# Performance work log

Measured on AMD Instinct MI355X. Metric: run time of the kernel, lower is better.

## Reference

```python
import jax, jax.numpy as jnp
import numpy as np

EPS = 1e-08


def setup_inputs() -> dict:
    key = jax.random.key(0)
    B, D = 8192, 512
    student_output = jax.random.normal(key, (B, D), dtype=jnp.float32)
    return {"student_output": student_output}


def reference(student_output) -> jnp.ndarray:
    # F.normalize(p=2, dim=-1, eps=EPS): x / max(||x||, eps)
    norm = jnp.linalg.norm(student_output, axis=-1, keepdims=True)
    x = student_output / jnp.maximum(norm, EPS)

    n = x.shape[0]
    # Pairwise inner products; mask the diagonal with -1 (self-match)
    dots = jnp.matmul(x, x.T)  # [B, B]
    idx = jnp.arange(n)
    dots = dots.at[idx, idx].set(-1.0)
    I = jnp.argmax(dots, axis=1)  # nearest neighbor index per row

    # torch.nn.PairwiseDistance(2, eps): ||x1 - x2 + eps||_2
    diff = x - x[I] + EPS
    distances = jnp.linalg.norm(diff, axis=-1)  # [B]
    loss = -jnp.mean(jnp.log(distances + EPS))
    return loss
```

## Files before the change

kernel.cpp:

```cpp
#include <hip/hip_runtime.h>
#include <hip/hip_bf16.h>
#include <math.h>

#define D_DIM 512
#define TM    128
#define TN    256

typedef int i32x4 __attribute__((ext_vector_type(4)));
typedef unsigned long long u64;


__device__ inline void async16(unsigned char* lds, const unsigned char* g) {
    __builtin_amdgcn_global_load_lds(
        (const __attribute__((address_space(1))) void*)g,
        (__attribute__((address_space(3))) void*)lds,
        16, 0, 0);
}


__global__ __launch_bounds__(256) void normalize_rows(
        const float* __restrict__ in, unsigned char* __restrict__ xb,
        float* __restrict__ inv_norm, u64* __restrict__ best,
        float* __restrict__ acc, int* __restrict__ cnt) {
    const int row  = blockIdx.x * 4 + (threadIdx.x >> 6);
    const int lane = threadIdx.x & 63;
    if (blockIdx.x == 0 && threadIdx.x == 0) { acc[0] = 0.f; cnt[0] = 0; }
    const float4* rp = (const float4*)(in + (size_t)row * D_DIM) + lane * 2;
    float4 a = rp[0], b = rp[1];
    float s = a.x*a.x + a.y*a.y + a.z*a.z + a.w*a.w
            + b.x*b.x + b.y*b.y + b.z*b.z + b.w*b.w;
    #pragma unroll
    for (int m = 1; m <= 32; m <<= 1) s += __shfl_xor(s, m, 64);
    float inv = 1.0f / fmaxf(sqrtf(s), 1e-8f);
    if (lane == 0) {
        inv_norm[row] = inv;
        best[row] = 0ull;
    }
    float sc = inv * 127.0f;
    int q0 = __float2int_rn(a.x*sc), q1 = __float2int_rn(a.y*sc);
    int q2 = __float2int_rn(a.z*sc), q3 = __float2int_rn(a.w*sc);
    int q4 = __float2int_rn(b.x*sc), q5 = __float2int_rn(b.y*sc);
    int q6 = __float2int_rn(b.z*sc), q7 = __float2int_rn(b.w*sc);
    int lo = (q0 & 255) | ((q1 & 255) << 8) | ((q2 & 255) << 16) | ((q3 & 255) << 24);
    int hi = (q4 & 255) | ((q5 & 255) << 8) | ((q6 & 255) << 16) | ((q7 & 255) << 24);
    ((int2*)(xb + (size_t)row * D_DIM))[lane] = make_int2(lo, hi);
}


__global__ __launch_bounds__(512, 4) void gemm_argmax(
        const unsigned char* __restrict__ X, u64* __restrict__ best) {
    __shared__ unsigned char smem[49152];
    unsigned char* As0 = smem;
    unsigned char* Bs0 = smem + 16384;
    unsigned int* rmerge = (unsigned int*)smem;
    unsigned int* cmerge = (unsigned int*)(smem + 2048);

    {
    }
    const int l    = blockIdx.x;
    const int x    = l & 7;
    const int rank = l >> 3;
    if (rank >= 132) return;
    int bi, bj;
    const int L0 = 2 * x + 2;
    if (rank < L0)                 { bj = x;      bi = rank; }
    else if (rank < 66)            { bj = 31 - x; bi = rank - L0; }
    else if (rank < 2 * x + 84)    { bj = x + 8;  bi = rank - 66; }
    else                           { bj = 23 - x; bi = rank - (2 * x + 84); }
    const int m0 = bi * TM;
    const int n0 = bj * TN;

    const int t    = threadIdx.x;
    const int lane = t & 63;
    const int w    = t >> 6;
    const int wm   = w >> 2;
    const int wn   = w & 3;
    const int qr   = lane & 15;
    const int quad = lane >> 4;

    const int srcsl = ((t & 3) ^ ((t >> 3) & 3)) * 16;
    const unsigned char* gA  = X + (size_t)(m0 + (t >> 2)) * D_DIM + srcsl;
    const unsigned char* gB  = X + (size_t)(n0 + (t >> 2)) * D_DIM + srcsl;
    const unsigned char* gB2 = gB + (size_t)128 * D_DIM;

    #define STAGE(buf, k0)                                        \
        do {                                                      \
            async16(As0 + (buf) * 8192 + t * 16, gA + (k0));      \
            async16(Bs0 + (buf) * 16384 + t * 16, gB + (k0));     \
            async16(Bs0 + (buf) * 16384 + 8192 + t * 16, gB2 + (k0)); \
        } while (0)

    i32x4 accm[4][4];
    #pragma unroll
    for (int mi = 0; mi < 4; mi++)
        #pragma unroll
        for (int ni = 0; ni < 4; ni++)
            accm[mi][ni] = (i32x4){0, 0, 0, 0};

    const int rdsl = (quad ^ ((qr >> 1) & 3)) * 16;

    STAGE(0, 0);
    #pragma unroll
    for (int t8 = 0; t8 < 8; t8++) {
        const int cur = t8 & 1;
        if (t8 < 7) {
            STAGE(cur ^ 1, (t8 + 1) * 64);
            asm volatile("s_waitcnt vmcnt(3)" ::: "memory");
        } else {
            asm volatile("s_waitcnt vmcnt(0)" ::: "memory");
        }
        __builtin_amdgcn_s_barrier();

        i32x4 av[4], bv[4];
        const unsigned char* pA = As0 + cur * 8192  + (wm * 64 + qr) * 64 + rdsl;
        const unsigned char* pB = Bs0 + cur * 16384 + (wn * 64 + qr) * 64 + rdsl;
        #pragma unroll
        for (int mi = 0; mi < 4; mi++)
            av[mi] = *(const i32x4*)(pA + mi * 1024);
        #pragma unroll
        for (int ni = 0; ni < 4; ni++)
            bv[ni] = *(const i32x4*)(pB + ni * 1024);
        #pragma unroll
        for (int mi = 0; mi < 4; mi++)
            #pragma unroll
            for (int ni = 0; ni < 4; ni++)
                accm[mi][ni] = __builtin_amdgcn_mfma_i32_16x16x64_i8(
                    av[mi], bv[ni], accm[mi][ni], 0, 0, 0);

        asm volatile("" ::: "memory");
        __builtin_amdgcn_s_barrier();
    }
    #undef STAGE

    const int colg_base = n0 + wn * 64 + qr;

    #pragma unroll
    for (int mi = 0; mi < 4; mi++) {
        #pragma unroll
        for (int r = 0; r < 4; r++) {
            const int rowl = wm * 64 + mi * 16 + quad * 4 + r;
            const int rowg = m0 + rowl;
            unsigned key = 0u;
            #pragma unroll
            for (int ni = 0; ni < 4; ni++) {
                const int colg = colg_base + ni * 16;
                const unsigned lcol = (unsigned)(wn * 64 + ni * 16 + qr);
                unsigned k = (((unsigned)accm[mi][ni][r] + 0x800000u) << 8)
                           | (255u - lcol);
                k = (colg == rowg) ? 0u : k;
                key = key > k ? key : k;
            }
            #pragma unroll
            for (int m = 1; m <= 8; m <<= 1) {
                unsigned o = (unsigned)__shfl_xor((int)key, m, 64);
                key = key > o ? key : o;
            }
            if (qr == 0) rmerge[rowl * 4 + wn] = key;
        }
    }

    #pragma unroll
    for (int ni = 0; ni < 4; ni++) {
        const int colg = colg_base + ni * 16;
        unsigned key = 0u;
        #pragma unroll
        for (int mi = 0; mi < 4; mi++) {
            #pragma unroll
            for (int r = 0; r < 4; r++) {
                const unsigned lrow = (unsigned)(wm * 64 + mi * 16 + quad * 4 + r);
                const int rowg = m0 + (int)lrow;
                unsigned k = (((unsigned)accm[mi][ni][r] + 0x800000u) << 8)
                           | (255u - lrow);
                k = (rowg == colg) ? 0u : k;
                key = key > k ? key : k;
            }
        }
        unsigned o = (unsigned)__shfl_xor((int)key, 16, 64);
        key = key > o ? key : o;
        o = (unsigned)__shfl_xor((int)key, 32, 64);
        key = key > o ? key : o;
        if (quad == 0) cmerge[(wn * 64 + ni * 16 + qr) * 2 + wm] = key;
    }
    __syncthreads();

    if (t < TM) {
        unsigned a0 = rmerge[t * 4], a1 = rmerge[t * 4 + 1];
        unsigned a2 = rmerge[t * 4 + 2], a3 = rmerge[t * 4 + 3];
        unsigned k01 = a0 > a1 ? a0 : a1;
        unsigned k23 = a2 > a3 ? a2 : a3;
        unsigned k = k01 > k23 ? k01 : k23;
        unsigned bd32 = (k >> 8) + 0x7F800000u;
        unsigned colg = (unsigned)(n0 + 255) - (k & 255u);
        u64 kk = ((u64)bd32 << 32) | (u64)(0xFFFFFFFFu - colg);
        atomicMax(&best[m0 + t], kk);
    }
    if (t < TN) {
        unsigned c0 = cmerge[t * 2], c1 = cmerge[t * 2 + 1];
        unsigned k = c0 > c1 ? c0 : c1;
        unsigned bd32 = (k >> 8) + 0x7F800000u;
        unsigned rowg = (unsigned)(m0 + 255) - (k & 255u);
        u64 kk = ((u64)bd32 << 32) | (u64)(0xFFFFFFFFu - rowg);
        atomicMax(&best[n0 + t], kk);
    }
}


__global__ __launch_bounds__(256) void neighbor_reduce(
        const float* __restrict__ in, const float* __restrict__ inv_norm,
        const u64* __restrict__ best, float* __restrict__ acc,
        int* __restrict__ cnt, float* __restrict__ out, int B) {
    const int wave = threadIdx.x >> 6;
    const int lane = threadIdx.x & 63;
    float lsum = 0.f;
    #pragma unroll
    for (int rr = 0; rr < 8; rr++) {
        const int row = blockIdx.x * 32 + wave * 8 + rr;
        u64 k   = best[row];
        int nbr = (int)(0xFFFFFFFFu - (unsigned)(k & 0xFFFFFFFFull));
        float ir  = inv_norm[row];
        float inb = inv_norm[nbr];
        const float4* rp = (const float4*)(in + (size_t)row * D_DIM) + lane * 2;
        const float4* np = (const float4*)(in + (size_t)nbr * D_DIM) + lane * 2;
        float4 r0 = rp[0], r1 = rp[1], q0 = np[0], q1 = np[1];
        float d0 = r0.x*ir - q0.x*inb + 1e-8f, d1 = r0.y*ir - q0.y*inb + 1e-8f;
        float d2 = r0.z*ir - q0.z*inb + 1e-8f, d3 = r0.w*ir - q0.w*inb + 1e-8f;
        float d4 = r1.x*ir - q1.x*inb + 1e-8f, d5 = r1.y*ir - q1.y*inb + 1e-8f;
        float d6 = r1.z*ir - q1.z*inb + 1e-8f, d7 = r1.w*ir - q1.w*inb + 1e-8f;
        float s = d0*d0 + d1*d1 + d2*d2 + d3*d3 + d4*d4 + d5*d5 + d6*d6 + d7*d7;
        #pragma unroll
        for (int m = 1; m <= 32; m <<= 1) s += __shfl_xor(s, m, 64);
        if (lane == 0) lsum += logf(sqrtf(s) + 1e-8f);
    }
    __shared__ float sb[4];
    if (lane == 0) sb[wave] = lsum;
    __syncthreads();
    if (threadIdx.x == 0) {
        float partial = sb[0] + sb[1] + sb[2] + sb[3];
        atomicAdd(acc, partial);
        __threadfence();
        int done = atomicAdd(cnt, 1);
        if (done == gridDim.x - 1) {
            __threadfence();
            float tot = atomicAdd(acc, 0.0f);
            out[0] = -tot / (float)B;
        }
    }
}


extern "C" void kernel_launch(void* const* d_in, const int* in_sizes, int n_in,
                              void* d_out, int out_size, void* d_ws, size_t ws_size,
                              hipStream_t stream) {
    const float* in = (const float*)d_in[0];
    const int B = in_sizes[0] / D_DIM;
    const int nblk = 144 * 8;

    char* w = (char*)d_ws;
    unsigned char* xb = (unsigned char*)w;
    float* invn = (float*)(w + (size_t)B * D_DIM);
    u64*   best = (u64*)(w + (size_t)B * D_DIM + (size_t)B * 4);
    float* acc  = (float*)(w + (size_t)B * D_DIM + (size_t)B * 4 + (size_t)B * 8);
    int*   cnt  = (int*)(acc + 1);
    float* out  = (float*)d_out;

    normalize_rows<<<B / 4, 256, 0, stream>>>(in, xb, invn, best, acc, cnt);
    gemm_argmax<<<nblk, 512, 0, stream>>>(xb, best);
    neighbor_reduce<<<B / 32, 256, 0, stream>>>(in, invn, best, acc, cnt, out, B);
}
```

Measured before the change: 108.3 us.

## Use square 256x256 symmetric tiles with k-blocked int8 layout and larger LDS stages

Result: slower. 119.6 us (+10.4%).

```diff
diff --git a/kernel.cpp b/kernel.cpp
--- a/kernel.cpp
+++ b/kernel.cpp
@@ -3,8 +3,7 @@
 #include <math.h>
 
 #define D_DIM 512
-#define TM    128
-#define TN    256
+#define TB    256
 
 typedef int i32x4 __attribute__((ext_vector_type(4)));
 typedef unsigned long long u64;
@@ -43,32 +42,31 @@
     int q6 = __float2int_rn(b.z*sc), q7 = __float2int_rn(b.w*sc);
     int lo = (q0 & 255) | ((q1 & 255) << 8) | ((q2 & 255) << 16) | ((q3 & 255) << 24);
     int hi = (q4 & 255) | ((q5 & 255) << 8) | ((q6 & 255) << 16) | ((q7 & 255) << 24);
-    ((int2*)(xb + (size_t)row * D_DIM))[lane] = make_int2(lo, hi);
-}
-
-
-__global__ __launch_bounds__(512, 4) void gemm_argmax(
+    unsigned char* dst = xb + (size_t)(lane >> 3) * 524288
+                            + (size_t)((lane >> 1) & 3) * 131072
+                            + (size_t)row * 16 + (lane & 1) * 8;
+    *(int2*)dst = make_int2(lo, hi);
+}
+
+
+__global__ __launch_bounds__(512, 2) void gemm_argmax(
         const unsigned char* __restrict__ X, u64* __restrict__ best) {
-    __shared__ unsigned char smem[49152];
-    unsigned char* As0 = smem;
-    unsigned char* Bs0 = smem + 16384;
+    __shared__ unsigned char smem[131072];
+    unsigned char* As = smem;
+    unsigned char* Bs = smem + 65536;
     unsigned int* rmerge = (unsigned int*)smem;
-    unsigned int* cmerge = (unsigned int*)(smem + 2048);
-
-    {
-    }
+    unsigned int* cmerge = (unsigned int*)(smem + 4096);
+
     const int l    = blockIdx.x;
     const int x    = l & 7;
     const int rank = l >> 3;
-    if (rank >= 132) return;
     int bi, bj;
-    const int L0 = 2 * x + 2;
-    if (rank < L0)                 { bj = x;      bi = rank; }
-    else if (rank < 66)            { bj = 31 - x; bi = rank - L0; }
-    else if (rank < 2 * x + 84)    { bj = x + 8;  bi = rank - 66; }
-    else                           { bj = 23 - x; bi = rank - (2 * x + 84); }
-    const int m0 = bi * TM;
-    const int n0 = bj * TN;
+    if (rank <= x)           { bj = x;      bi = rank; }
+    else if (rank < 33)      { bj = 31 - x; bi = rank - (x + 1); }
+    else if (rank < 42 + x)  { bj = x + 8;  bi = rank - 33; }
+    else                     { bj = 23 - x; bi = rank - (42 + x); }
+    const int m0 = bi * TB;
+    const int n0 = bj * TB;
 
     const int t    = threadIdx.x;
     const int lane = t & 63;
@@ -78,54 +76,68 @@
     const int qr   = lane & 15;
     const int quad = lane >> 4;
 
-    const int srcsl = ((t & 3) ^ ((t >> 3) & 3)) * 16;
-    const unsigned char* gA  = X + (size_t)(m0 + (t >> 2)) * D_DIM + srcsl;
-    const unsigned char* gB  = X + (size_t)(n0 + (t >> 2)) * D_DIM + srcsl;
-    const unsigned char* gB2 = gB + (size_t)128 * D_DIM;
-
-    #define STAGE(buf, k0)                                        \
-        do {                                                      \
-            async16(As0 + (buf) * 8192 + t * 16, gA + (k0));      \
-            async16(Bs0 + (buf) * 16384 + t * 16, gB + (k0));     \
-            async16(Bs0 + (buf) * 16384 + 8192 + t * 16, gB2 + (k0)); \
+    const int tl = t & 255;
+    const int th = t >> 8;
+
+    #define STAGE(buf, t4)                                                  \
+        do {                                                                \
+            _Pragma("unroll")                                               \
+            for (int j = 0; j < 4; j++) {                                   \
+                const int e = 2 * j + th;                                   \
+                async16(As + (buf) * 32768 + e * 4096 + tl * 16,            \
+                        X + (size_t)(2 * (t4) + (e >> 2)) * 524288          \
+                          + (size_t)(e & 3) * 131072                        \
+                          + (size_t)m0 * 16 + tl * 16);                     \
+            }                                                               \
+            _Pragma("unroll")                                               \
+            for (int j = 0; j < 4; j++) {                                   \
+                const int e = 2 * j + th;                                   \
+                async16(Bs + (buf) * 32768 + e * 4096 + tl * 16,            \
+                        X + (size_t)(2 * (t4) + (e >> 2)) * 524288          \
+                          + (size_t)(e & 3) * 131072                        \
+                          + (size_t)n0 * 16 + tl * 16);                     \
+            }                                                               \
         } while (0)
 
-    i32x4 accm[4][4];
-    #pragma unroll
-    for (int mi = 0; mi < 4; mi++)
+    i32x4 accm[8][4];
+    #pragma unroll
+    for (int mi = 0; mi < 8; mi++)
         #pragma unroll
         for (int ni = 0; ni < 4; ni++)
             accm[mi][ni] = (i32x4){0, 0, 0, 0};
 
-    const int rdsl = (quad ^ ((qr >> 1) & 3)) * 16;
-
     STAGE(0, 0);
     #pragma unroll
-    for (int t8 = 0; t8 < 8; t8++) {
-        const int cur = t8 & 1;
-        if (t8 < 7) {
-            STAGE(cur ^ 1, (t8 + 1) * 64);
-            asm volatile("s_waitcnt vmcnt(3)" ::: "memory");
+    for (int t4 = 0; t4 < 4; t4++) {
+        const int buf = t4 & 1;
+        if (t4 < 3) {
+            STAGE(buf ^ 1, t4 + 1);
+            asm volatile("s_waitcnt vmcnt(16)" ::: "memory");
         } else {
             asm volatile("s_waitcnt vmcnt(0)" ::: "memory");
         }
         __builtin_amdgcn_s_barrier();
 
-        i32x4 av[4], bv[4];
-        const unsigned char* pA = As0 + cur * 8192  + (wm * 64 + qr) * 64 + rdsl;
-        const unsigned char* pB = Bs0 + cur * 16384 + (wn * 64 + qr) * 64 + rdsl;
-        #pragma unroll
-        for (int mi = 0; mi < 4; mi++)
-            av[mi] = *(const i32x4*)(pA + mi * 1024);
-        #pragma unroll
-        for (int ni = 0; ni < 4; ni++)
-            bv[ni] = *(const i32x4*)(pB + ni * 1024);
-        #pragma unroll
-        for (int mi = 0; mi < 4; mi++)
+        #pragma unroll
+        for (int ks = 0; ks < 2; ks++) {
+            const unsigned char* pA = As + buf * 32768 + ks * 16384
+                                    + quad * 4096 + (wm * 128 + qr) * 16;
+            const unsigned char* pB = Bs + buf * 32768 + ks * 16384
+                                    + quad * 4096 + (wn * 64 + qr) * 16;
+            i32x4 av[8], bv[4];
+            #pragma unroll
+            for (int mi = 0; mi < 8; mi++)
+                av[mi] = *(const i32x4*)(pA + mi * 256);
             #pragma unroll
             for (int ni = 0; ni < 4; ni++)
-                accm[mi][ni] = __builtin_amdgcn_mfma_i32_16x16x64_i8(
-                    av[mi], bv[ni], accm[mi][ni], 0, 0, 0);
+                bv[ni] = *(const i32x4*)(pB + ni * 256);
+            #pragma unroll
+            for (int mi = 0; mi < 8; mi++)
+                #pragma unroll
+                for (int ni = 0; ni < 4; ni++)
+                    accm[mi][ni] = __builtin_amdgcn_mfma_i32_16x16x64_i8(
+                        av[mi], bv[ni], accm[mi][ni], 0, 0, 0);
+        }
 
         asm volatile("" ::: "memory");
         __builtin_amdgcn_s_barrier();
@@ -135,10 +147,10 @@
     const int colg_base = n0 + wn * 64 + qr;
 
     #pragma unroll
-    for (int mi = 0; mi < 4; mi++) {
+    for (int mi = 0; mi < 8; mi++) {
         #pragma unroll
         for (int r = 0; r < 4; r++) {
-            const int rowl = wm * 64 + mi * 16 + quad * 4 + r;
+            const int rowl = wm * 128 + mi * 16 + quad * 4 + r;
             const int rowg = m0 + rowl;
             unsigned key = 0u;
             #pragma unroll
@@ -164,10 +176,10 @@
         const int colg = colg_base + ni * 16;
         unsigned key = 0u;
         #pragma unroll
-        for (int mi = 0; mi < 4; mi++) {
+        for (int mi = 0; mi < 8; mi++) {
             #pragma unroll
             for (int r = 0; r < 4; r++) {
-                const unsigned lrow = (unsigned)(wm * 64 + mi * 16 + quad * 4 + r);
+                const unsigned lrow = (unsigned)(wm * 128 + mi * 16 + quad * 4 + r);
                 const int rowg = m0 + (int)lrow;
                 unsigned k = (((unsigned)accm[mi][ni][r] + 0x800000u) << 8)
                            | (255u - lrow);
@@ -183,7 +195,7 @@
     }
     __syncthreads();
 
-    if (t < TM) {
+    if (t < TB) {
         unsigned a0 = rmerge[t * 4], a1 = rmerge[t * 4 + 1];
         unsigned a2 = rmerge[t * 4 + 2], a3 = rmerge[t * 4 + 3];
         unsigned k01 = a0 > a1 ? a0 : a1;
@@ -193,14 +205,14 @@
         unsigned colg = (unsigned)(n0 + 255) - (k & 255u);
         u64 kk = ((u64)bd32 << 32) | (u64)(0xFFFFFFFFu - colg);
         atomicMax(&best[m0 + t], kk);
-    }
-    if (t < TN) {
-        unsigned c0 = cmerge[t * 2], c1 = cmerge[t * 2 + 1];
+    } else {
+        const int tt = t - TB;
+        unsigned c0 = cmerge[tt * 2], c1 = cmerge[tt * 2 + 1];
         unsigned k = c0 > c1 ? c0 : c1;
         unsigned bd32 = (k >> 8) + 0x7F800000u;
         unsigned rowg = (unsigned)(m0 + 255) - (k & 255u);
         u64 kk = ((u64)bd32 << 32) | (u64)(0xFFFFFFFFu - rowg);
-        atomicMax(&best[n0 + t], kk);
+        atomicMax(&best[n0 + tt], kk);
     }
 }
 
@@ -253,7 +265,7 @@
                               hipStream_t stream) {
     const float* in = (const float*)d_in[0];
     const int B = in_sizes[0] / D_DIM;
-    const int nblk = 144 * 8;
+    const int nblk = 528;
 
     char* w = (char*)d_ws;
     unsigned char* xb = (unsigned char*)w;
```

## Enlarge GEMM-argmax tiles to 256x256 with 1024-thread blocks

Applied to the files above, without the earlier changes.

Result: slower. 122.0 us (+12.7%).

```diff
diff --git a/kernel.cpp b/kernel.cpp
--- a/kernel.cpp
+++ b/kernel.cpp
@@ -3,8 +3,7 @@
 #include <math.h>
 
 #define D_DIM 512
-#define TM    128
-#define TN    256
+#define TB    256
 
 typedef int i32x4 __attribute__((ext_vector_type(4)));
 typedef unsigned long long u64;
@@ -47,28 +46,23 @@
 }
 
 
-__global__ __launch_bounds__(512, 4) void gemm_argmax(
+__global__ __launch_bounds__(1024, 1) void gemm_argmax(
         const unsigned char* __restrict__ X, u64* __restrict__ best) {
-    __shared__ unsigned char smem[49152];
-    unsigned char* As0 = smem;
-    unsigned char* Bs0 = smem + 16384;
-    unsigned int* rmerge = (unsigned int*)smem;
-    unsigned int* cmerge = (unsigned int*)(smem + 2048);
-
-    {
-    }
+    __shared__ unsigned char As[2][16384];
+    __shared__ unsigned char Bs[2][16384];
+    __shared__ unsigned int rmerge[TB * 4];
+    __shared__ unsigned int cmerge[TB * 4];
+
     const int l    = blockIdx.x;
     const int x    = l & 7;
     const int rank = l >> 3;
-    if (rank >= 132) return;
     int bi, bj;
-    const int L0 = 2 * x + 2;
-    if (rank < L0)                 { bj = x;      bi = rank; }
-    else if (rank < 66)            { bj = 31 - x; bi = rank - L0; }
-    else if (rank < 2 * x + 84)    { bj = x + 8;  bi = rank - 66; }
-    else                           { bj = 23 - x; bi = rank - (2 * x + 84); }
-    const int m0 = bi * TM;
-    const int n0 = bj * TN;
+    if (rank <= x)           { bj = x;      bi = rank; }
+    else if (rank < 33)      { bj = 31 - x; bi = rank - (x + 1); }
+    else if (rank < 42 + x)  { bj = x + 8;  bi = rank - 33; }
+    else                     { bj = 23 - x; bi = rank - (42 + x); }
+    const int m0 = bi * TB;
+    const int n0 = bj * TB;
 
     const int t    = threadIdx.x;
     const int lane = t & 63;
@@ -79,15 +73,13 @@
     const int quad = lane >> 4;
 
     const int srcsl = ((t & 3) ^ ((t >> 3) & 3)) * 16;
-    const unsigned char* gA  = X + (size_t)(m0 + (t >> 2)) * D_DIM + srcsl;
-    const unsigned char* gB  = X + (size_t)(n0 + (t >> 2)) * D_DIM + srcsl;
-    const unsigned char* gB2 = gB + (size_t)128 * D_DIM;
-
-    #define STAGE(buf, k0)                                        \
-        do {                                                      \
-            async16(As0 + (buf) * 8192 + t * 16, gA + (k0));      \
-            async16(Bs0 + (buf) * 16384 + t * 16, gB + (k0));     \
-            async16(Bs0 + (buf) * 16384 + 8192 + t * 16, gB2 + (k0)); \
+    const unsigned char* gA = X + (size_t)(m0 + (t >> 2)) * D_DIM + srcsl;
+    const unsigned char* gB = X + (size_t)(n0 + (t >> 2)) * D_DIM + srcsl;
+
+    #define STAGE(buf, k0)                              \
+        do {                                            \
+            async16(&As[buf][t * 16], gA + (k0));       \
+            async16(&Bs[buf][t * 16], gB + (k0));       \
         } while (0)
 
     i32x4 accm[4][4];
@@ -101,19 +93,19 @@
 
     STAGE(0, 0);
     #pragma unroll
-    for (int t8 = 0; t8 < 8; t8++) {
-        const int cur = t8 & 1;
-        if (t8 < 7) {
-            STAGE(cur ^ 1, (t8 + 1) * 64);
-            asm volatile("s_waitcnt vmcnt(3)" ::: "memory");
+    for (int kt = 0; kt < 8; kt++) {
+        const int cur = kt & 1;
+        if (kt < 7) {
+            STAGE(cur ^ 1, (kt + 1) * 64);
+            asm volatile("s_waitcnt vmcnt(2)" ::: "memory");
         } else {
             asm volatile("s_waitcnt vmcnt(0)" ::: "memory");
         }
         __builtin_amdgcn_s_barrier();
 
         i32x4 av[4], bv[4];
-        const unsigned char* pA = As0 + cur * 8192  + (wm * 64 + qr) * 64 + rdsl;
-        const unsigned char* pB = Bs0 + cur * 16384 + (wn * 64 + qr) * 64 + rdsl;
+        const unsigned char* pA = &As[cur][(wm * 64 + qr) * 64 + rdsl];
+        const unsigned char* pB = &Bs[cur][(wn * 64 + qr) * 64 + rdsl];
         #pragma unroll
         for (int mi = 0; mi < 4; mi++)
             av[mi] = *(const i32x4*)(pA + mi * 1024);
@@ -179,11 +171,11 @@
         key = key > o ? key : o;
         o = (unsigned)__shfl_xor((int)key, 32, 64);
         key = key > o ? key : o;
-        if (quad == 0) cmerge[(wn * 64 + ni * 16 + qr) * 2 + wm] = key;
+        if (quad == 0) cmerge[(wn * 64 + ni * 16 + qr) * 4 + wm] = key;
     }
     __syncthreads();
 
-    if (t < TM) {
+    if (t < TB) {
         unsigned a0 = rmerge[t * 4], a1 = rmerge[t * 4 + 1];
         unsigned a2 = rmerge[t * 4 + 2], a3 = rmerge[t * 4 + 3];
         unsigned k01 = a0 > a1 ? a0 : a1;
@@ -193,14 +185,17 @@
         unsigned colg = (unsigned)(n0 + 255) - (k & 255u);
         u64 kk = ((u64)bd32 << 32) | (u64)(0xFFFFFFFFu - colg);
         atomicMax(&best[m0 + t], kk);
-    }
-    if (t < TN) {
-        unsigned c0 = cmerge[t * 2], c1 = cmerge[t * 2 + 1];
-        unsigned k = c0 > c1 ? c0 : c1;
+    } else if (t < 2 * TB) {
+        const int tt = t - TB;
+        unsigned c0 = cmerge[tt * 4], c1 = cmerge[tt * 4 + 1];
+        unsigned c2 = cmerge[tt * 4 + 2], c3 = cmerge[tt * 4 + 3];
+        unsigned k01 = c0 > c1 ? c0 : c1;
+        unsigned k23 = c2 > c3 ? c2 : c3;
+        unsigned k = k01 > k23 ? k01 : k23;
         unsigned bd32 = (k >> 8) + 0x7F800000u;
         unsigned rowg = (unsigned)(m0 + 255) - (k & 255u);
         u64 kk = ((u64)bd32 << 32) | (u64)(0xFFFFFFFFu - rowg);
-        atomicMax(&best[n0 + t], kk);
+        atomicMax(&best[n0 + tt], kk);
     }
 }
 
@@ -253,7 +248,7 @@
                               hipStream_t stream) {
     const float* in = (const float*)d_in[0];
     const int B = in_sizes[0] / D_DIM;
-    const int nblk = 144 * 8;
+    const int nblk = 528;
 
     char* w = (char*)d_ws;
     unsigned char* xb = (unsigned char*)w;
@@ -264,6 +259,6 @@
     float* out  = (float*)d_out;
 
     normalize_rows<<<B / 4, 256, 0, stream>>>(in, xb, invn, best, acc, cnt);
-    gemm_argmax<<<nblk, 512, 0, stream>>>(xb, best);
+    gemm_argmax<<<nblk, 1024, 0, stream>>>(xb, best);
     neighbor_reduce<<<B / 32, 256, 0, stream>>>(in, invn, best, acc, cnt, out, B);
 }
```

## Triple-buffer LDS in int8 GEMM-argmax with interleaved loads and MFMA priority

Applied to the files above, without the earlier changes.

After: 106.2 us (median of 2 runs). No clear change (-1.9%).

```diff
diff --git a/kernel.cpp b/kernel.cpp
--- a/kernel.cpp
+++ b/kernel.cpp
@@ -15,6 +15,18 @@
         (const __attribute__((address_space(1))) void*)g,
         (__attribute__((address_space(3))) void*)lds,
         16, 0, 0);
+}
+
+__device__ inline bool decode_tile(int l, int& bi, int& bj) {
+    const int x    = l & 7;
+    const int rank = l >> 3;
+    if (rank >= 132) return false;
+    const int L0 = 2 * x + 2;
+    if (rank < L0)              { bj = x;      bi = rank; }
+    else if (rank < 66)         { bj = 31 - x; bi = rank - L0; }
+    else if (rank < 2 * x + 84) { bj = x + 8;  bi = rank - 66; }
+    else                        { bj = 23 - x; bi = rank - (2 * x + 84); }
+    return true;
 }
 
 
@@ -49,24 +61,14 @@
 
 __global__ __launch_bounds__(512, 4) void gemm_argmax(
         const unsigned char* __restrict__ X, u64* __restrict__ best) {
-    __shared__ unsigned char smem[49152];
+    __shared__ unsigned char smem[73728];
     unsigned char* As0 = smem;
-    unsigned char* Bs0 = smem + 16384;
+    unsigned char* Bs0 = smem + 24576;
     unsigned int* rmerge = (unsigned int*)smem;
     unsigned int* cmerge = (unsigned int*)(smem + 2048);
 
-    {
-    }
-    const int l    = blockIdx.x;
-    const int x    = l & 7;
-    const int rank = l >> 3;
-    if (rank >= 132) return;
     int bi, bj;
-    const int L0 = 2 * x + 2;
-    if (rank < L0)                 { bj = x;      bi = rank; }
-    else if (rank < 66)            { bj = 31 - x; bi = rank - L0; }
-    else if (rank < 2 * x + 84)    { bj = x + 8;  bi = rank - 66; }
-    else                           { bj = 23 - x; bi = rank - (2 * x + 84); }
+    if (!decode_tile(blockIdx.x, bi, bj)) return;
     const int m0 = bi * TM;
     const int n0 = bj * TN;
 
@@ -83,13 +85,6 @@
     const unsigned char* gB  = X + (size_t)(n0 + (t >> 2)) * D_DIM + srcsl;
     const unsigned char* gB2 = gB + (size_t)128 * D_DIM;
 
-    #define STAGE(buf, k0)                                        \
-        do {                                                      \
-            async16(As0 + (buf) * 8192 + t * 16, gA + (k0));      \
-            async16(Bs0 + (buf) * 16384 + t * 16, gB + (k0));     \
-            async16(Bs0 + (buf) * 16384 + 8192 + t * 16, gB2 + (k0)); \
-        } while (0)
-
     i32x4 accm[4][4];
     #pragma unroll
     for (int mi = 0; mi < 4; mi++)
@@ -99,38 +94,65 @@
 
     const int rdsl = (quad ^ ((qr >> 1) & 3)) * 16;
 
-    STAGE(0, 0);
+    async16(As0 + t * 16,         gA);
+    async16(Bs0 + t * 16,         gB);
+    async16(Bs0 + 8192 + t * 16,  gB2);
+    async16(As0 + 8192 + t * 16,         gA + 64);
+    async16(Bs0 + 16384 + t * 16,        gB + 64);
+    async16(Bs0 + 16384 + 8192 + t * 16, gB2 + 64);
+    asm volatile("s_waitcnt vmcnt(3)" ::: "memory");
+    __builtin_amdgcn_s_barrier();
+
     #pragma unroll
     for (int t8 = 0; t8 < 8; t8++) {
-        const int cur = t8 & 1;
-        if (t8 < 7) {
-            STAGE(cur ^ 1, (t8 + 1) * 64);
+        const int cur = t8 % 3;
+        const int nxt = (t8 + 2) % 3;
+        const int k2  = (t8 + 2) * 64;
+        const unsigned char* pA = As0 + cur * 8192  + (wm * 64 + qr) * 64 + rdsl;
+        const unsigned char* pB = Bs0 + cur * 16384 + (wn * 64 + qr) * 64 + rdsl;
+
+        i32x4 av[4], bv[4];
+        #pragma unroll
+        for (int mi = 0; mi < 4; mi++)
+            av[mi] = *(const i32x4*)(pA + mi * 1024);
+        bv[0] = *(const i32x4*)(pB);
+        bv[1] = *(const i32x4*)(pB + 1024);
+        if (t8 < 6) {
+            async16(As0 + nxt * 8192 + t * 16,  gA + k2);
+            async16(Bs0 + nxt * 16384 + t * 16, gB + k2);
+        }
+        __builtin_amdgcn_s_setprio(1);
+        #pragma unroll
+        for (int mi = 0; mi < 4; mi++) {
+            accm[mi][0] = __builtin_amdgcn_mfma_i32_16x16x64_i8(
+                av[mi], bv[0], accm[mi][0], 0, 0, 0);
+            accm[mi][1] = __builtin_amdgcn_mfma_i32_16x16x64_i8(
+                av[mi], bv[1], accm[mi][1], 0, 0, 0);
+        }
+        __builtin_amdgcn_s_setprio(0);
+
+        bv[2] = *(const i32x4*)(pB + 2048);
+        bv[3] = *(const i32x4*)(pB + 3072);
+        if (t8 < 6)
+            async16(Bs0 + nxt * 16384 + 8192 + t * 16, gB2 + k2);
+        __builtin_amdgcn_s_setprio(1);
+        #pragma unroll
+        for (int mi = 0; mi < 4; mi++) {
+            accm[mi][2] = __builtin_amdgcn_mfma_i32_16x16x64_i8(
+                av[mi], bv[2], accm[mi][2], 0, 0, 0);
+            accm[mi][3] = __builtin_amdgcn_mfma_i32_16x16x64_i8(
+                av[mi], bv[3], accm[mi][3], 0, 0, 0);
+        }
+        __builtin_amdgcn_s_setprio(0);
+
+        asm volatile("" ::: "memory");
+        if (t8 < 6) {
             asm volatile("s_waitcnt vmcnt(3)" ::: "memory");
         } else {
             asm volatile("s_waitcnt vmcnt(0)" ::: "memory");
         }
         __builtin_amdgcn_s_barrier();
-
-        i32x4 av[4], bv[4];
-        const unsigned char* pA = As0 + cur * 8192  + (wm * 64 + qr) * 64 + rdsl;
-        const unsigned char* pB = Bs0 + cur * 16384 + (wn * 64 + qr) * 64 + rdsl;
-        #pragma unroll
-        for (int mi = 0; mi < 4; mi++)
-            av[mi] = *(const i32x4*)(pA + mi * 1024);
-        #pragma unroll
-        for (int ni = 0; ni < 4; ni++)
-            bv[ni] = *(const i32x4*)(pB + ni * 1024);
-        #pragma unroll
-        for (int mi = 0; mi < 4; mi++)
-            #pragma unroll
-            for (int ni = 0; ni < 4; ni++)
-                accm[mi][ni] = __builtin_amdgcn_mfma_i32_16x16x64_i8(
-                    av[mi], bv[ni], accm[mi][ni], 0, 0, 0);
-
-        asm volatile("" ::: "memory");
-        __builtin_amdgcn_s_barrier();
-    }
-    #undef STAGE
+    }
 
     const int colg_base = n0 + wn * 64 + qr;
 
```
